# Optimization experiments

Measured on AMD Instinct MI355X. Metric: run time of the kernel, lower is better.

Reference implementation:

```python
import jax, jax.numpy as jnp
import numpy as np

N = 100000   # nodes
E = 300000   # directed edges (avg degree 3, molecular graphs)
G = 4000     # molecules in the batch
IN = 9
HID = 128
HEADS = 4
NEG_SLOPE = 0.2


def setup_inputs() -> dict:
    key = jax.random.key(0)
    ks = jax.random.split(key, 12)
    x = jax.random.normal(ks[0], (N, IN), dtype=jnp.float32)
    edge_index = jax.random.randint(ks[1], (2, E), 0, N, dtype=jnp.int32)
    batch = jnp.sort(jax.random.randint(ks[2], (N,), 0, G, dtype=jnp.int32))
    s = 0.1  # keep activations in a sane range
    W1 = jax.random.normal(ks[3], (IN, HEADS * HID), dtype=jnp.float32) * s
    a_src1 = jax.random.normal(ks[4], (HEADS, HID), dtype=jnp.float32) * s
    a_dst1 = jax.random.normal(ks[5], (HEADS, HID), dtype=jnp.float32) * s
    b1 = jax.random.normal(ks[6], (HEADS * HID,), dtype=jnp.float32) * s
    W2 = jax.random.normal(ks[7], (HEADS * HID, HID), dtype=jnp.float32) * s
    a_src2 = jax.random.normal(ks[8], (1, HID), dtype=jnp.float32) * s
    a_dst2 = jax.random.normal(ks[9], (1, HID), dtype=jnp.float32) * s
    b2 = jax.random.normal(ks[10], (HID,), dtype=jnp.float32) * s
    return {"x": x, "edge_index": edge_index, "batch": batch,
            "W1": W1, "a_src1": a_src1, "a_dst1": a_dst1, "b1": b1,
            "W2": W2, "a_src2": a_src2, "a_dst2": a_dst2, "b2": b2}


def _gat_conv(x, edge_index, W, a_src, a_dst, b, heads, out_ch, concat):
    """PyG GATConv: linear proj, per-edge leaky-relu attention logits,
    segment softmax over destination nodes, scatter-add aggregation.
    add_self_loops=True (PyG default)."""
    n = x.shape[0]
    loops = jnp.arange(n, dtype=edge_index.dtype)
    src = jnp.concatenate([edge_index[0], loops])
    dst = jnp.concatenate([edge_index[1], loops])

    h = (x @ W).reshape(n, heads, out_ch)                  # [N, H, C]
    alpha_s = jnp.einsum('nhc,hc->nh', h, a_src)           # [N, H]
    alpha_d = jnp.einsum('nhc,hc->nh', h, a_dst)           # [N, H]

    logits = jax.nn.leaky_relu(alpha_s[src] + alpha_d[dst], NEG_SLOPE)  # [Etot, H]
    # numerically stable segment softmax over incoming edges of each dst
    m = jax.ops.segment_max(logits, dst, num_segments=n)   # [N, H] (finite: self-loops)
    e = jnp.exp(logits - m[dst])
    z = jax.ops.segment_sum(e, dst, num_segments=n)
    alpha = e / (z[dst] + 1e-16)                           # [Etot, H]

    msg = h[src] * alpha[:, :, None]                       # [Etot, H, C]
    out = jax.ops.segment_sum(msg, dst, num_segments=n)    # [N, H, C]
    if concat:
        out = out.reshape(n, heads * out_ch)
    else:
        out = out.mean(axis=1)
    return out + b


def reference(x, edge_index, batch, W1, a_src1, a_dst1, b1, W2, a_src2, a_dst2, b2):
    h = jax.nn.elu(_gat_conv(x, edge_index, W1, a_src1, a_dst1, b1, HEADS, HID, True))
    h = jax.nn.elu(_gat_conv(h, edge_index, W2, a_src2, a_dst2, b2, 1, HID, True))
    # global mean pool per graph
    sums = jax.ops.segment_sum(h, batch, num_segments=G)   # [G, HID]
    cnt = jax.ops.segment_sum(jnp.ones((h.shape[0],), h.dtype), batch, num_segments=G)
    return sums / jnp.maximum(cnt, 1.0)[:, None]
```

## Files before the change

### kernel.cpp

```cpp
#include <hip/hip_runtime.h>

#define N_NODES 100000
#define N_EDGES 300000
#define N_GRAPHS 4000
#define CAP 32

typedef float f32x4 __attribute__((ext_vector_type(4)));
typedef __bf16 bf16x8 __attribute__((ext_vector_type(8)));
typedef __bf16 bf16x2 __attribute__((ext_vector_type(2)));

static const size_t OFF_XA    = 0;
static const size_t OFF_AD4   = OFF_XA + (size_t)N_NODES * 16;
static const size_t OFF_P2B   = OFF_AD4 + (size_t)N_NODES * 4;
static const size_t OFF_ASAD2 = OFF_P2B + (size_t)N_NODES * 64;
static const size_t OFF_WSB   = OFF_ASAD2 + (size_t)N_NODES * 2;
static const size_t OFF_INVC  = OFF_WSB + 32768;
static const size_t OFF_INT   = OFF_INVC + 4096;

#define PRE_NODE_END 391
#define PRE_PACKB_END 455
#define PRE_DEG_END 846
#define PRE_OUT_END 1346
#define PRE_INV_END 1362

__device__ __forceinline__ float lrelu(float x) { return x < 0.f ? 0.2f * x : x; }
__device__ __forceinline__ float elu(float x)   { return x > 0.f ? x : __expf(x) - 1.f; }

__global__ __launch_bounds__(256) void k_pre(
    const float* __restrict__ x, const float* __restrict__ W1,
    const float* __restrict__ a_src1, const float* __restrict__ a_dst1,
    const float* __restrict__ W2, const int* __restrict__ batch,
    float* __restrict__ xa, float* __restrict__ ad4,
    __bf16* __restrict__ wsB, int* __restrict__ deg, float* __restrict__ out,
    float* __restrict__ inv_cnt) {
    int b = blockIdx.x, tid = threadIdx.x;
    if (b < PRE_NODE_END) {
        __shared__ float wf[72];
        if (tid < 72) {
            int isd = tid / 36, r = tid % 36, k = r / 4, h = r % 4;
            const float* a = isd ? a_dst1 : a_src1;
            float s = 0.f;
            for (int c = 0; c < 128; c++) s += W1[k * 512 + h * 128 + c] * a[h * 128 + c];
            wf[tid] = s;
        }
        __syncthreads();
        int n = b * 256 + tid;
        if (n >= N_NODES) return;
        float xv[9];
#pragma unroll
        for (int k = 0; k < 9; k++) xv[k] = x[n * 9 + k];
        float as[4], ad[4];
#pragma unroll
        for (int h = 0; h < 4; h++) {
            float s = 0.f, d = 0.f;
#pragma unroll
            for (int k = 0; k < 9; k++) {
                s += xv[k] * wf[k * 4 + h];
                d += xv[k] * wf[36 + k * 4 + h];
            }
            as[h] = s; ad[h] = d;
        }
        f32x4* xp = (f32x4*)(xa + (size_t)n * 16);
        xp[0] = (f32x4){xv[0], xv[1], xv[2], xv[3]};
        xp[1] = (f32x4){xv[4], xv[5], xv[6], xv[7]};
        xp[2] = (f32x4){xv[8], as[0], as[1], as[2]};
        xp[3] = (f32x4){as[3], 0.f, 0.f, 0.f};
        *(f32x4*)(ad4 + (size_t)n * 4) = (f32x4){ad[0], ad[1], ad[2], ad[3]};
    } else if (b < PRE_PACKB_END) {
        int t = (b - PRE_NODE_END) * 256 + tid;
#pragma unroll
        for (int m = 0; m < 4; m++) {
            int idx = t * 4 + m;
            int k = idx >> 7, nn = idx & 127;
            wsB[(size_t)nn * 512 + k] = (__bf16)W2[(size_t)k * 128 + nn];
        }
    } else if (b < PRE_DEG_END) {
        int idx = (b - PRE_PACKB_END) * 256 + tid;
        if (idx < N_NODES) deg[idx] = 0;
    } else if (b < PRE_OUT_END) {
        int idx = (b - PRE_DEG_END) * 256 + tid;
        if (idx < 128000) ((f32x4*)out)[idx] = (f32x4){0.f, 0.f, 0.f, 0.f};
    } else {
        int g = (b - PRE_OUT_END) * 256 + tid;
        if (g >= N_GRAPHS) return;
        int lo = 0, hi = N_NODES;
        while (lo < hi) { int mid = (lo + hi) >> 1; if (batch[mid] < g) lo = mid + 1; else hi = mid; }
        int s = lo; hi = N_NODES;
        while (lo < hi) { int mid = (lo + hi) >> 1; if (batch[mid] < g + 1) lo = mid + 1; else hi = mid; }
        int c = lo - s;
        inv_cnt[g] = 1.f / (float)(c > 0 ? c : 1);
    }
}

__global__ void k_bucket(const int* __restrict__ ei, int* __restrict__ deg,
                         int* __restrict__ bucket) {
    int e = blockIdx.x * 256 + threadIdx.x;
    if (e >= N_EDGES) return;
    int s = ei[e], d = ei[N_EDGES + e];
    int slot = atomicAdd(&deg[d], 1);
    if (slot < CAP) bucket[d * CAP + slot] = s;
}

__global__ __launch_bounds__(512, 6) void k_gemm(
    const float* __restrict__ xa, const float* __restrict__ ad4,
    const int* __restrict__ deg, const int* __restrict__ bucket,
    const float* __restrict__ W1, const float* __restrict__ b1,
    const __bf16* __restrict__ wsB,
    const float* __restrict__ a_src2, const float* __restrict__ a_dst2,
    __bf16* __restrict__ p2b, float* __restrict__ asad2) {
    __shared__ __bf16 As[64 * 256];
    __shared__ __bf16 AgT[64 * 72];
    __shared__ float red2[64 * 16];
    const int tid = threadIdx.x;
    const int lane = tid & 63;
    const int w = tid >> 6;
    const int i = lane & 15;
    const int q = lane >> 4;
    const int m0 = blockIdx.x * 64;

    {
        int nh = tid >> 1, sub = tid & 1;
        int r = nh >> 2, h = nh & 3;
        int n = m0 + r;
        float acc[9] = {};
        float z = 0.f;
        bool valid = (n < N_NODES);
        if (valid) {
            float ad = ad4[(size_t)n * 4 + h];
            int dg = deg[n];
            if (dg > CAP) dg = CAP;
            if (sub == 0) {
                const f32x4* xp = (const f32x4*)(xa + (size_t)n * 16);
                f32x4 v0 = xp[0], v1 = xp[1], v2 = xp[2], v3 = xp[3];
                float asl = (h == 0) ? v2.y : (h == 1) ? v2.z : (h == 2) ? v2.w : v3.x;
                float e = __expf(lrelu(asl + ad));
                z += e;
                acc[0] += e * v0.x; acc[1] += e * v0.y; acc[2] += e * v0.z; acc[3] += e * v0.w;
                acc[4] += e * v1.x; acc[5] += e * v1.y; acc[6] += e * v1.z; acc[7] += e * v1.w;
                acc[8] += e * v2.x;
            }
            for (int j = sub; j < dg; j += 2) {
                int src = bucket[n * CAP + j];
                const f32x4* xp = (const f32x4*)(xa + (size_t)src * 16);
                f32x4 v0 = xp[0], v1 = xp[1], v2 = xp[2], v3 = xp[3];
                float asl = (h == 0) ? v2.y : (h == 1) ? v2.z : (h == 2) ? v2.w : v3.x;
                float e = __expf(lrelu(asl + ad));
                z += e;
                acc[0] += e * v0.x; acc[1] += e * v0.y; acc[2] += e * v0.z; acc[3] += e * v0.w;
                acc[4] += e * v1.x; acc[5] += e * v1.y; acc[6] += e * v1.z; acc[7] += e * v1.w;
                acc[8] += e * v2.x;
            }
        }
        z += __shfl_xor(z, 1);
#pragma unroll
        for (int k = 0; k < 9; k++) acc[k] += __shfl_xor(acc[k], 1);
        if (sub == 0) {
            float inv = valid ? 1.f / z : 0.f;
            bf16x8 p0;
#pragma unroll
            for (int k = 0; k < 8; k++) p0[k] = (__bf16)(acc[k] * inv);
            __bf16* dst = AgT + r * 72 + h * 16;
            *(bf16x8*)dst = p0;
            dst[8] = (__bf16)(acc[8] * inv);
        }
    }
    __syncthreads();

    f32x4 acc[4];
#pragma unroll
    for (int r = 0; r < 4; r++) acc[r] = (f32x4){0.f, 0.f, 0.f, 0.f};

    const int row = tid & 63;
    const int kg = __builtin_amdgcn_readfirstlane(tid >> 6);
    const int rt_p1 = row >> 4, il = row & 15;
    const __bf16* bcol = wsB + (size_t)(w * 16 + i) * 512 + q * 8;

#pragma unroll
    for (int half = 0; half < 2; half++) {
        bf16x8 breg[8];
#pragma unroll
        for (int kc = 0; kc < 8; kc++)
            breg[kc] = *(const bf16x8*)(bcol + half * 256 + kc * 32);

        {
            int h = half * 2 + (kg >> 2);
            float ag[9];
            {
                bf16x8 a8 = *(const bf16x8*)&AgT[row * 72 + h * 16];
#pragma unroll
                for (int k = 0; k < 8; k++) ag[k] = (float)a8[k];
                ag[8] = (float)AgT[row * 72 + h * 16 + 8];
            }
#pragma unroll
            for (int c8 = 0; c8 < 4; c8++) {
                int j0 = half * 256 + kg * 32 + c8 * 8;
                float o[8];
#pragma unroll
                for (int e = 0; e < 8; e++) o[e] = b1[j0 + e];
#pragma unroll
                for (int k = 0; k < 9; k++) {
                    const float* wp = &W1[k * 512 + j0];
#pragma unroll
                    for (int e = 0; e < 8; e++) o[e] += ag[k] * wp[e];
                }
                bf16x8 pk;
#pragma unroll
                for (int e = 0; e < 8; e++) pk[e] = (__bf16)elu(o[e]);
                *(bf16x8*)&As[(rt_p1 * 8 + kg) * 512 + (c8 * 16 + il) * 8] = pk;
            }
        }
        __syncthreads();

#pragma unroll
        for (int kc = 0; kc < 8; kc++) {
#pragma unroll
            for (int rt = 0; rt < 4; rt++) {
                bf16x8 af = *(const bf16x8*)&As[(rt * 8 + kc) * 512 + lane * 8];
                acc[rt] = __builtin_amdgcn_mfma_f32_16x16x32_bf16(af, breg[kc], acc[rt], 0, 0, 0);
            }
        }
        __syncthreads();
    }

    float as2 = a_src2[w * 16 + i];
    float ad2 = a_dst2[w * 16 + i];
#pragma unroll
    for (int rt = 0; rt < 4; rt++) {
#pragma unroll
        for (int qq = 0; qq < 4; qq++) {
            int r2 = rt * 16 + q * 4 + qq;
            float v = acc[rt][qq];
            if (m0 + r2 < N_NODES)
                p2b[(size_t)(m0 + r2) * 128 + w * 16 + i] = (__bf16)v;
            float s = v * as2, d = v * ad2;
#pragma unroll
            for (int off = 1; off < 16; off <<= 1) {
                s += __shfl_xor(s, off);
                d += __shfl_xor(d, off);
            }
            if (i == 0) {
                red2[r2 * 16 + w * 2] = s;
                red2[r2 * 16 + w * 2 + 1] = d;
            }
        }
    }
    __syncthreads();
    if (tid < 128) {
        int r2 = tid >> 1, cc = tid & 1;
        float sum = 0.f;
#pragma unroll
        for (int ww = 0; ww < 8; ww++) sum += red2[r2 * 16 + ww * 2 + cc];
        if (m0 + r2 < N_NODES) asad2[(size_t)(m0 + r2) * 2 + cc] = sum;
    }
}

__global__ void k_agg2_pool(const __bf16* __restrict__ p2b, const float* __restrict__ asad2,
                            const int* __restrict__ deg, const int* __restrict__ bucket,
                            const float* __restrict__ b2, const int* __restrict__ batch,
                            const float* __restrict__ inv_cnt, float* __restrict__ out) {
    int wv = (blockIdx.x * 256 + threadIdx.x) >> 6;
    wv = __builtin_amdgcn_readfirstlane(wv);
    int lane = threadIdx.x & 63;
    int nbase = wv * 8;
    if (nbase >= N_NODES) return;
    int nend = nbase + 8;
    if (nend > N_NODES) nend = N_NODES;
    float b2a = b2[2 * lane], b2b = b2[2 * lane + 1];
    float g0 = 0.f, g1 = 0.f;
    int curg = batch[nbase];
    for (int n = nbase; n < nend; n++) {
        float ad = asad2[n * 2 + 1];
        float e = __expf(lrelu(asad2[n * 2] + ad));
        float z = e;
        bf16x2 v = ((const bf16x2*)(p2b + (size_t)n * 128))[lane];
        float a0 = e * (float)v.x;
        float a1 = e * (float)v.y;
        int dg = deg[n];
        if (dg > CAP) dg = CAP;
        for (int j = 0; j < dg; j++) {
            int s = bucket[n * CAP + j];
            float e2 = __expf(lrelu(asad2[s * 2] + ad));
            z += e2;
            bf16x2 sv = ((const bf16x2*)(p2b + (size_t)s * 128))[lane];
            a0 += e2 * (float)sv.x;
            a1 += e2 * (float)sv.y;
        }
        float inv = 1.f / z;
        float o0 = elu(a0 * inv + b2a);
        float o1 = elu(a1 * inv + b2b);
        int g = batch[n];
        if (g != curg) {
            float ic = inv_cnt[curg];
            atomicAdd(&out[(size_t)curg * 128 + 2 * lane], g0 * ic);
            atomicAdd(&out[(size_t)curg * 128 + 2 * lane + 1], g1 * ic);
            g0 = 0.f; g1 = 0.f; curg = g;
        }
        g0 += o0; g1 += o1;
    }
    float ic = inv_cnt[curg];
    atomicAdd(&out[(size_t)curg * 128 + 2 * lane], g0 * ic);
    atomicAdd(&out[(size_t)curg * 128 + 2 * lane + 1], g1 * ic);
}

extern "C" void kernel_launch(void* const* d_in, const int* in_sizes, int n_in,
                              void* d_out, int out_size, void* d_ws, size_t ws_size,
                              hipStream_t stream) {
    const float* x       = (const float*)d_in[0];
    const int*   ei      = (const int*)d_in[1];
    const int*   batch   = (const int*)d_in[2];
    const float* W1      = (const float*)d_in[3];
    const float* a_src1  = (const float*)d_in[4];
    const float* a_dst1  = (const float*)d_in[5];
    const float* b1      = (const float*)d_in[6];
    const float* W2      = (const float*)d_in[7];
    const float* a_src2  = (const float*)d_in[8];
    const float* a_dst2  = (const float*)d_in[9];
    const float* b2      = (const float*)d_in[10];
    float* out = (float*)d_out;

    float* wsf   = (float*)d_ws;
    float* xa    = wsf + OFF_XA;
    float* ad4   = wsf + OFF_AD4;
    __bf16* p2b  = (__bf16*)(wsf + OFF_P2B);
    float* asad2 = wsf + OFF_ASAD2;
    __bf16* wsB  = (__bf16*)(wsf + OFF_WSB);
    float* invc  = wsf + OFF_INVC;
    int* wsi    = (int*)(wsf + OFF_INT);
    int* deg    = wsi;
    int* bucket = wsi + N_NODES;

    k_pre<<<PRE_INV_END, 256, 0, stream>>>(x, W1, a_src1, a_dst1, W2, batch,
                                           xa, ad4, wsB, deg, out, invc);
    k_bucket<<<(N_EDGES + 255) / 256, 256, 0, stream>>>(ei, deg, bucket);
    k_gemm<<<(N_NODES + 63) / 64, 512, 0, stream>>>(xa, ad4, deg, bucket, W1, b1,
                                                    wsB, a_src2, a_dst2, p2b, asad2);
    k_agg2_pool<<<((N_NODES + 7) / 8 * 64 + 255) / 256, 256, 0, stream>>>(
        p2b, asad2, deg, bucket, b2, batch, invc, out);
}
```

Measured before the change: 217.0 us.

## Stage W1 in LDS for layer-1 recompute and use one wave per node in agg2

In k_gemm, each half of W1 (9x256 floats, padded rows) is staged into shared memory and read with vector loads, replacing scattered global loads inside the layer-1 recompute. red2 now aliases AgT so the extra LDS fits. k_agg2_pool switches from 8 nodes per wave with per-graph partial sums to one wave per node. Its neighbor loop is unrolled by 4 to expose more independent gathers, at the cost of one pair of atomicAdds per node instead of per graph run.

Measured after the change: 269.2 us. +24.0%, slower.

```diff
diff --git a/kernel.cpp b/kernel.cpp
--- a/kernel.cpp
+++ b/kernel.cpp
@@ -109,14 +109,20 @@
     const float* __restrict__ a_src2, const float* __restrict__ a_dst2,
     __bf16* __restrict__ p2b, float* __restrict__ asad2) {
     __shared__ __bf16 As[64 * 256];
+    __shared__ float W1s[9 * 260];
     __shared__ __bf16 AgT[64 * 72];
-    __shared__ float red2[64 * 16];
+    float* red2 = (float*)AgT;
     const int tid = threadIdx.x;
     const int lane = tid & 63;
     const int w = tid >> 6;
     const int i = lane & 15;
     const int q = lane >> 4;
     const int m0 = blockIdx.x * 64;
+
+    for (int idx = tid; idx < 2304; idx += 512) {
+        int k = idx >> 8, j = idx & 255;
+        W1s[k * 260 + j] = W1[k * 512 + j];
+    }
 
     {
         int nh = tid >> 1, sub = tid & 1;
@@ -193,15 +199,19 @@
             }
 #pragma unroll
             for (int c8 = 0; c8 < 4; c8++) {
-                int j0 = half * 256 + kg * 32 + c8 * 8;
+                int jr = kg * 32 + c8 * 8;
+                int j0 = half * 256 + jr;
                 float o[8];
 #pragma unroll
                 for (int e = 0; e < 8; e++) o[e] = b1[j0 + e];
 #pragma unroll
                 for (int k = 0; k < 9; k++) {
-                    const float* wp = &W1[k * 512 + j0];
-#pragma unroll
-                    for (int e = 0; e < 8; e++) o[e] += ag[k] * wp[e];
+                    f32x4 wa = *(const f32x4*)&W1s[k * 260 + jr];
+                    f32x4 wb = *(const f32x4*)&W1s[k * 260 + jr + 4];
+                    o[0] += ag[k] * wa.x; o[1] += ag[k] * wa.y;
+                    o[2] += ag[k] * wa.z; o[3] += ag[k] * wa.w;
+                    o[4] += ag[k] * wb.x; o[5] += ag[k] * wb.y;
+                    o[6] += ag[k] * wb.z; o[7] += ag[k] * wb.w;
                 }
                 bf16x8 pk;
 #pragma unroll
@@ -210,6 +220,13 @@
             }
         }
         __syncthreads();
+
+        if (half == 0) {
+            for (int idx = tid; idx < 2304; idx += 512) {
+                int k = idx >> 8, j = idx & 255;
+                W1s[k * 260 + j] = W1[k * 512 + 256 + j];
+            }
+        }
 
 #pragma unroll
         for (int kc = 0; kc < 8; kc++) {
@@ -258,48 +275,42 @@
                             const int* __restrict__ deg, const int* __restrict__ bucket,
                             const float* __restrict__ b2, const int* __restrict__ batch,
                             const float* __restrict__ inv_cnt, float* __restrict__ out) {
-    int wv = (blockIdx.x * 256 + threadIdx.x) >> 6;
-    wv = __builtin_amdgcn_readfirstlane(wv);
+    int n = (blockIdx.x * 256 + threadIdx.x) >> 6;
+    n = __builtin_amdgcn_readfirstlane(n);
     int lane = threadIdx.x & 63;
-    int nbase = wv * 8;
-    if (nbase >= N_NODES) return;
-    int nend = nbase + 8;
-    if (nend > N_NODES) nend = N_NODES;
-    float b2a = b2[2 * lane], b2b = b2[2 * lane + 1];
-    float g0 = 0.f, g1 = 0.f;
-    int curg = batch[nbase];
-    for (int n = nbase; n < nend; n++) {
-        float ad = asad2[n * 2 + 1];
-        float e = __expf(lrelu(asad2[n * 2] + ad));
-        float z = e;
-        bf16x2 v = ((const bf16x2*)(p2b + (size_t)n * 128))[lane];
-        float a0 = e * (float)v.x;
-        float a1 = e * (float)v.y;
-        int dg = deg[n];
-        if (dg > CAP) dg = CAP;
-        for (int j = 0; j < dg; j++) {
-            int s = bucket[n * CAP + j];
-            float e2 = __expf(lrelu(asad2[s * 2] + ad));
-            z += e2;
-            bf16x2 sv = ((const bf16x2*)(p2b + (size_t)s * 128))[lane];
-            a0 += e2 * (float)sv.x;
-            a1 += e2 * (float)sv.y;
-        }
-        float inv = 1.f / z;
-        float o0 = elu(a0 * inv + b2a);
-        float o1 = elu(a1 * inv + b2b);
-        int g = batch[n];
-        if (g != curg) {
-            float ic = inv_cnt[curg];
-            atomicAdd(&out[(size_t)curg * 128 + 2 * lane], g0 * ic);
-            atomicAdd(&out[(size_t)curg * 128 + 2 * lane + 1], g1 * ic);
-            g0 = 0.f; g1 = 0.f; curg = g;
-        }
-        g0 += o0; g1 += o1;
-    }
-    float ic = inv_cnt[curg];
-    atomicAdd(&out[(size_t)curg * 128 + 2 * lane], g0 * ic);
-    atomicAdd(&out[(size_t)curg * 128 + 2 * lane + 1], g1 * ic);
+    if (n >= N_NODES) return;
+    float ad = asad2[n * 2 + 1];
+    float e = __expf(lrelu(asad2[n * 2] + ad));
+    float z = e;
+    bf16x2 v = ((const bf16x2*)(p2b + (size_t)n * 128))[lane];
+    float a0 = e * (float)v.x;
+    float a1 = e * (float)v.y;
+    int dg = deg[n];
+    if (dg > CAP) dg = CAP;
+    for (int j = 0; j < dg; j += 4) {
+        int s0 = bucket[n * CAP + j];
+        int s1 = bucket[n * CAP + min(j + 1, dg - 1)];
+        int s2 = bucket[n * CAP + min(j + 2, dg - 1)];
+        int s3 = bucket[n * CAP + min(j + 3, dg - 1)];
+        float l0 = asad2[s0 * 2], l1 = asad2[s1 * 2];
+        float l2 = asad2[s2 * 2], l3 = asad2[s3 * 2];
+        bf16x2 w0 = ((const bf16x2*)(p2b + (size_t)s0 * 128))[lane];
+        bf16x2 w1 = ((const bf16x2*)(p2b + (size_t)s1 * 128))[lane];
+        bf16x2 w2 = ((const bf16x2*)(p2b + (size_t)s2 * 128))[lane];
+        bf16x2 w3 = ((const bf16x2*)(p2b + (size_t)s3 * 128))[lane];
+        float e0 = __expf(lrelu(l0 + ad));
+        float e1 = (j + 1 < dg) ? __expf(lrelu(l1 + ad)) : 0.f;
+        float e2 = (j + 2 < dg) ? __expf(lrelu(l2 + ad)) : 0.f;
+        float e3 = (j + 3 < dg) ? __expf(lrelu(l3 + ad)) : 0.f;
+        z += e0 + e1 + e2 + e3;
+        a0 += e0 * (float)w0.x + e1 * (float)w1.x + e2 * (float)w2.x + e3 * (float)w3.x;
+        a1 += e0 * (float)w0.y + e1 * (float)w1.y + e2 * (float)w2.y + e3 * (float)w3.y;
+    }
+    float inv = 1.f / z;
+    int g = batch[n];
+    float ic = inv_cnt[g];
+    atomicAdd(&out[(size_t)g * 128 + 2 * lane], elu(a0 * inv + b2[2 * lane]) * ic);
+    atomicAdd(&out[(size_t)g * 128 + 2 * lane + 1], elu(a1 * inv + b2[2 * lane + 1]) * ic);
 }
 
 extern "C" void kernel_launch(void* const* d_in, const int* in_sizes, int n_in,
@@ -334,6 +345,6 @@
     k_bucket<<<(N_EDGES + 255) / 256, 256, 0, stream>>>(ei, deg, bucket);
     k_gemm<<<(N_NODES + 63) / 64, 512, 0, stream>>>(xa, ad4, deg, bucket, W1, b1,
                                                     wsB, a_src2, a_dst2, p2b, asad2);
-    k_agg2_pool<<<((N_NODES + 7) / 8 * 64 + 255) / 256, 256, 0, stream>>>(
+    k_agg2_pool<<<((size_t)N_NODES * 64 + 255) / 256, 256, 0, stream>>>(
         p2b, asad2, deg, bucket, b2, batch, invc, out);
 }
```
